# Kernel tuning notes

Measured on AMD Instinct MI355X. Metric: run time of the kernel, lower is better.

## Reference

```python
import jax, jax.numpy as jnp
import numpy as np

NEG = float(-2**32 + 1)  # huge negative used by the original sign-based masking
EPS = 1e-8
NUM_BLOCKS = 3
NUM_HEADS = 1


def _mha(xq, xk, xv, Wq, bq, Wk, bk, Wv, bv):
    # manual QKV with ReLU, as in the torch module
    Q = jax.nn.relu(xq @ Wq + bq)   # [B, Lq, D]
    K = jax.nn.relu(xk @ Wk + bk)   # [B, Lk, D]
    V = jax.nn.relu(xv @ Wv + bv)
    B, Lq, D = Q.shape
    Lk = K.shape[1]
    dh = D // NUM_HEADS
    Qh = Q.reshape(B, Lq, NUM_HEADS, dh)
    Kh = K.reshape(B, Lk, NUM_HEADS, dh)
    Vh = V.reshape(B, Lk, NUM_HEADS, dh)
    scores = jnp.einsum('bqhd,bkhd->bhqk', Qh, Kh) / jnp.sqrt(jnp.float32(dh))
    # sign-based key padding mask (rows whose embedding-sum is exactly 0)
    key_mask0 = (jnp.sign(jnp.abs(jnp.sum(xk, axis=-1))) == 0.0).astype(scores.dtype)  # [B, Lk]
    cond = key_mask0[:, None, None, :]
    scores = NEG * cond + scores * (1.0 - cond)
    attn = jax.nn.softmax(scores, axis=-1)
    # post-softmax query mask
    qmask = jnp.sign(jnp.abs(jnp.sum(xq, axis=-1)))  # [B, Lq]
    attn = attn * qmask[:, None, :, None]
    out = jnp.einsum('bhqk,bkhd->bqhd', attn, Vh).reshape(B, Lq, D)
    return out + xq  # residual; note: the torch mha never applies its layernorm


def _layernorm(x, g, b):
    mu = jnp.mean(x, axis=-1, keepdims=True)
    var = jnp.mean(jnp.square(x - mu), axis=-1, keepdims=True)
    return (x - mu) / jnp.sqrt(var + EPS) * g + b


def _ffn(x, W1, b1, W2, b2, g, bln):
    h = jax.nn.relu(x @ W1 + b1) @ W2 + b2
    return _layernorm(h, g, bln) + x


def setup_inputs() -> dict:
    key = jax.random.key(0)
    ks = jax.random.split(key, 9)
    B, L, V, D, NB = 4096, 50, 50000, 200, NUM_BLOCKS
    tokens = jax.random.randint(ks[0], (B, L), 0, V)
    emb = jax.random.normal(ks[1], (V, D), dtype=jnp.float32) * 0.1
    emb = emb.at[0].set(0.0)  # padding token row -> triggers sign masks
    s = 1.0 / np.sqrt(D)
    Wq = jax.random.normal(ks[2], (NB, D, D), dtype=jnp.float32) * s
    Wk = jax.random.normal(ks[3], (NB, D, D), dtype=jnp.float32) * s
    Wv = jax.random.normal(ks[4], (NB, D, D), dtype=jnp.float32) * s
    W1 = jax.random.normal(ks[5], (NB, D, D), dtype=jnp.float32) * s
    W2 = jax.random.normal(ks[6], (NB, D, D), dtype=jnp.float32) * s
    z = jnp.zeros((NB, D), dtype=jnp.float32)
    return dict(tokens=tokens, emb=emb,
                Wq=Wq, bq=z, Wk=Wk, bk=z, Wv=Wv, bv=z,
                W1=W1, b1=z, W2=W2, b2=z,
                ln_g=jnp.ones((NB, D), dtype=jnp.float32), ln_b=z)


def reference(tokens, emb, Wq, bq, Wk, bk, Wv, bv, W1, b1, W2, b2, ln_g, ln_b):
    x = emb[tokens]  # [B, L, D]
    for i in range(NUM_BLOCKS):
        x = _mha(x, x, x, Wq[i], bq[i], Wk[i], bk[i], Wv[i], bv[i])
        x = _ffn(x, W1[i], b1[i], W2[i], b2[i], ln_g[i], ln_b[i])
    return x
```

## Files before the change

### kernel.cpp

```cpp
#include <hip/hip_runtime.h>
#include <hip/hip_bf16.h>
#include <math.h>

#define LQ 50
#define DD 200
#define NBLK 3
#define NT 1024
#define NW 16

#define KC 13
#define NT32 7
#define MAT_U (KC * NT32 * 128)

#define APS 408
#define VTS 72
#define PS  136
#define SS  66

#define NEGC (-4294967295.0f)
#define SCALE 0.07071067811865475f

typedef __attribute__((ext_vector_type(4)))  float f32x4;
typedef __attribute__((ext_vector_type(16))) float f32x16;
typedef __attribute__((ext_vector_type(8)))  short s16x8;

__device__ __forceinline__ unsigned short bf16_rne(float x) {
  unsigned u = __float_as_uint(x);
  unsigned r = u + 0x7FFF + ((u >> 16) & 1);
  return (unsigned short)(r >> 16);
}
__device__ __forceinline__ float bf16_f(unsigned short h) {
  return __uint_as_float((unsigned)h << 16);
}
__device__ __forceinline__ void splitf(float x, short& h, short& l) {
  __hip_bfloat16 bh = __float2bfloat16(x);
  float hf = __bfloat162float(bh);
  __hip_bfloat16 bl = __float2bfloat16(x - hf);
  h = (short)__builtin_bit_cast(unsigned short, bh);
  l = (short)__builtin_bit_cast(unsigned short, bl);
}
__device__ __forceinline__ unsigned short bfbits(float x) {
  __hip_bfloat16 bh = __float2bfloat16(x);
  return __builtin_bit_cast(unsigned short, bh);
}
__device__ __forceinline__ float joinf(short h, short l) {
  return __bfloat162float(__builtin_bit_cast(__hip_bfloat16, (unsigned short)h)) +
         __bfloat162float(__builtin_bit_cast(__hip_bfloat16, (unsigned short)l));
}

__device__ __forceinline__ float wave_sum(float v) {
  #pragma unroll
  for (int off = 32; off > 0; off >>= 1) v += __shfl_xor(v, off, 64);
  return v;
}
__device__ __forceinline__ float wave_max(float v) {
  #pragma unroll
  for (int off = 32; off > 0; off >>= 1) v = fmaxf(v, __shfl_xor(v, off, 64));
  return v;
}

__global__ __launch_bounds__(64)
void swizzle_w(const float* __restrict__ Wq, const float* __restrict__ Wk,
               const float* __restrict__ Wv, const float* __restrict__ W1,
               const float* __restrict__ W2, unsigned short* __restrict__ wbuf)
{
  int t = blockIdx.x;
  int nt = t % NT32; t /= NT32;
  int kc = t % KC;  t /= KC;
  int mat = t;
  int layer = mat / 5, which = mat % 5;
  const float* W;
  switch (which) {
    case 0: W = Wq; break;
    case 1: W = Wk; break;
    case 2: W = Wv; break;
    case 3: W = W1; break;
    default: W = W2; break;
  }
  W += (size_t)layer * DD * DD;

  const int l = threadIdx.x;
  const int n = nt * 32 + (l & 31);
  const int kb = kc * 16 + (l >> 5) * 8;
  s16x8 vh, vl;
  #pragma unroll
  for (int j = 0; j < 8; ++j) {
    int k = kb + j;
    float w = (k < DD && n < DD) ? W[k * DD + n] : 0.0f;
    unsigned short h = bf16_rne(w);
    unsigned short lo = bf16_rne(w - bf16_f(h));
    vh[j] = (short)h;
    vl[j] = (short)lo;
  }
  size_t base = ((size_t)((mat * KC + kc) * NT32 + nt)) * 1024 + l * 8;
  *(s16x8*)(wbuf + base)       = vh;
  *(s16x8*)(wbuf + base + 512) = vl;
}

__device__ __forceinline__ void mm32_ct_pair(
    const short* __restrict__ srcp, const s16x8* __restrict__ wt,
    const float* __restrict__ bias, short* __restrict__ dstp, int nt, int lane)
{
  const int h = lane >> 5, l31 = lane & 31;
  f32x16 acc0 = (f32x16)0.f, acc1 = (f32x16)0.f;
  int r1 = 32 + l31; if (r1 >= LQ) r1 = 0;
  const short* arow0 = srcp + l31 * APS;
  const short* arow1 = srcp + r1 * APS;

  #pragma unroll 1
  for (int kc = 0; kc < KC; ++kc) {
    const s16x8* wp = wt + (size_t)(kc * NT32 + nt) * 128 + lane;
    s16x8 wh = wp[0], wl = wp[64];
    const int ch = 2 * kc + h;
    const bool ok = (ch < 25);
    {
      s16x8 ah = (s16x8)0, al = (s16x8)0;
      if (ok) { const short* p = arow0 + ch * 16; ah = *(const s16x8*)p; al = *(const s16x8*)(p + 8); }
      acc0 = __builtin_amdgcn_mfma_f32_32x32x16_bf16(wh, ah, acc0, 0, 0, 0);
      acc0 = __builtin_amdgcn_mfma_f32_32x32x16_bf16(wh, al, acc0, 0, 0, 0);
      acc0 = __builtin_amdgcn_mfma_f32_32x32x16_bf16(wl, ah, acc0, 0, 0, 0);
    }
    {
      s16x8 ah = (s16x8)0, al = (s16x8)0;
      if (ok) { const short* p = arow1 + ch * 16; ah = *(const s16x8*)p; al = *(const s16x8*)(p + 8); }
      acc1 = __builtin_amdgcn_mfma_f32_32x32x16_bf16(wh, ah, acc1, 0, 0, 0);
      acc1 = __builtin_amdgcn_mfma_f32_32x32x16_bf16(wh, al, acc1, 0, 0, 0);
      acc1 = __builtin_amdgcn_mfma_f32_32x32x16_bf16(wl, ah, acc1, 0, 0, 0);
    }
  }

  #pragma unroll
  for (int rt = 0; rt < 2; ++rt) {
    const int r = rt * 32 + l31;
    if (r < LQ) {
      #pragma unroll
      for (int q2 = 0; q2 < 4; ++q2) {
        const int nb = nt * 32 + 8 * q2 + 4 * h;
        if (nb + 3 < DD) {
          float4 bv = *(const float4*)(bias + nb);
          float v0 = fmaxf((rt ? acc1[q2*4+0] : acc0[q2*4+0]) + bv.x, 0.f);
          float v1 = fmaxf((rt ? acc1[q2*4+1] : acc0[q2*4+1]) + bv.y, 0.f);
          float v2 = fmaxf((rt ? acc1[q2*4+2] : acc0[q2*4+2]) + bv.z, 0.f);
          float v3 = fmaxf((rt ? acc1[q2*4+3] : acc0[q2*4+3]) + bv.w, 0.f);
          short h0,l0,h1,l1,h2,l2,h3,l3;
          splitf(v0,h0,l0); splitf(v1,h1,l1); splitf(v2,h2,l2); splitf(v3,h3,l3);
          uint2 ph, pl;
          ph.x = (unsigned short)h0 | ((unsigned)(unsigned short)h1 << 16);
          ph.y = (unsigned short)h2 | ((unsigned)(unsigned short)h3 << 16);
          pl.x = (unsigned short)l0 | ((unsigned)(unsigned short)l1 << 16);
          pl.y = (unsigned short)l2 | ((unsigned)(unsigned short)l3 << 16);
          short* base = dstp + r * APS + (nb >> 3) * 16 + (nb & 7);
          *(uint2*)base = ph;
          *(uint2*)(base + 8) = pl;
        }
      }
    }
  }
}

__device__ __forceinline__ void mm32_v(
    const short* __restrict__ srcp, const s16x8* __restrict__ wt,
    const float* __restrict__ bias, short* __restrict__ vtp, int nt, int lane)
{
  const int h = lane >> 5, l31 = lane & 31;
  f32x16 acc0 = (f32x16)0.f, acc1 = (f32x16)0.f;
  int r1 = 32 + l31; if (r1 >= LQ) r1 = 0;
  const short* arow0 = srcp + l31 * APS;
  const short* arow1 = srcp + r1 * APS;

  #pragma unroll 1
  for (int kc = 0; kc < KC; ++kc) {
    const s16x8* wp = wt + (size_t)(kc * NT32 + nt) * 128 + lane;
    s16x8 wh = wp[0], wl = wp[64];
    const int ch = 2 * kc + h;
    const bool ok = (ch < 25);
    {
      s16x8 ah = (s16x8)0, al = (s16x8)0;
      if (ok) { const short* p = arow0 + ch * 16; ah = *(const s16x8*)p; al = *(const s16x8*)(p + 8); }
      acc0 = __builtin_amdgcn_mfma_f32_32x32x16_bf16(ah, wh, acc0, 0, 0, 0);
      acc0 = __builtin_amdgcn_mfma_f32_32x32x16_bf16(al, wh, acc0, 0, 0, 0);
      acc0 = __builtin_amdgcn_mfma_f32_32x32x16_bf16(ah, wl, acc0, 0, 0, 0);
    }
    {
      s16x8 ah = (s16x8)0, al = (s16x8)0;
      if (ok) { const short* p = arow1 + ch * 16; ah = *(const s16x8*)p; al = *(const s16x8*)(p + 8); }
      acc1 = __builtin_amdgcn_mfma_f32_32x32x16_bf16(ah, wh, acc1, 0, 0, 0);
      acc1 = __builtin_amdgcn_mfma_f32_32x32x16_bf16(al, wh, acc1, 0, 0, 0);
      acc1 = __builtin_amdgcn_mfma_f32_32x32x16_bf16(ah, wl, acc1, 0, 0, 0);
    }
  }

  const int d = nt * 32 + l31;
  if (d < DD) {
    const float bvs = bias[d];
    #pragma unroll
    for (int mt2 = 0; mt2 < 2; ++mt2) {
      #pragma unroll
      for (int q2 = 0; q2 < 4; ++q2) {
        const int rb = mt2 * 32 + 8 * q2 + 4 * h;
        float vv[4];
        #pragma unroll
        for (int e = 0; e < 4; ++e) {
          const int r = rb + e;
          float v = (mt2 ? acc1[q2*4+e] : acc0[q2*4+e]) + bvs;
          vv[e] = (r < LQ) ? fmaxf(v, 0.f) : 0.f;
        }
        uint2 pk;
        pk.x = (unsigned)bfbits(vv[0]) | ((unsigned)bfbits(vv[1]) << 16);
        pk.y = (unsigned)bfbits(vv[2]) | ((unsigned)bfbits(vv[3]) << 16);
        *(uint2*)(vtp + d * VTS + (rb >> 3) * 8 + (rb & 7)) = pk;
      }
    }
  }
}

__device__ __forceinline__ void mm32_w1(
    const short* __restrict__ srcp, const s16x8* __restrict__ wt,
    const float* __restrict__ bias, short* __restrict__ dstp,
    int nt, int rt, int lane)
{
  const int h = lane >> 5, l31 = lane & 31;
  f32x16 acc = (f32x16)0.f;
  int r = rt * 32 + l31;
  int rr = (r >= LQ) ? 0 : r;
  const short* arow = srcp + rr * APS;

  const s16x8* wp = wt + (size_t)nt * 128 + lane;
  s16x8 wh = wp[0], wl = wp[64];
  #pragma unroll 1
  for (int kc = 0; kc < KC; ++kc) {
    s16x8 nh = (s16x8)0, nl = (s16x8)0;
    if (kc + 1 < KC) {
      const s16x8* np = wt + (size_t)((kc + 1) * NT32 + nt) * 128 + lane;
      nh = np[0]; nl = np[64];
    }
    const int ch = 2 * kc + h;
    s16x8 ah = (s16x8)0, al = (s16x8)0;
    if (ch < 25) { const short* p = arow + ch * 16; ah = *(const s16x8*)p; al = *(const s16x8*)(p + 8); }
    acc = __builtin_amdgcn_mfma_f32_32x32x16_bf16(wh, ah, acc, 0, 0, 0);
    acc = __builtin_amdgcn_mfma_f32_32x32x16_bf16(wh, al, acc, 0, 0, 0);
    acc = __builtin_amdgcn_mfma_f32_32x32x16_bf16(wl, ah, acc, 0, 0, 0);
    wh = nh; wl = nl;
  }

  if (r < LQ) {
    #pragma unroll
    for (int q2 = 0; q2 < 4; ++q2) {
      const int nb = nt * 32 + 8 * q2 + 4 * h;
      if (nb + 3 < DD) {
        float4 bv = *(const float4*)(bias + nb);
        float v0 = fmaxf(acc[q2*4+0] + bv.x, 0.f);
        float v1 = fmaxf(acc[q2*4+1] + bv.y, 0.f);
        float v2 = fmaxf(acc[q2*4+2] + bv.z, 0.f);
        float v3 = fmaxf(acc[q2*4+3] + bv.w, 0.f);
        uint2 ph;
        ph.x = (unsigned)bfbits(v0) | ((unsigned)bfbits(v1) << 16);
        ph.y = (unsigned)bfbits(v2) | ((unsigned)bfbits(v3) << 16);
        *(uint2*)(dstp + r * APS + (nb >> 3) * 16 + (nb & 7)) = ph;
      }
    }
  }
}

__device__ __forceinline__ void mm32_w2(
    const short* __restrict__ srcp, const s16x8* __restrict__ wt,
    const float* __restrict__ bias, float* __restrict__ dstf,
    int nt, int rt, int lane)
{
  const int h = lane >> 5, l31 = lane & 31;
  f32x16 acc = (f32x16)0.f;
  int r = rt * 32 + l31;
  int rr = (r >= LQ) ? 0 : r;
  const short* arow = srcp + rr * APS;

  const s16x8* wp = wt + (size_t)nt * 128 + lane;
  s16x8 wh = wp[0], wl = wp[64];
  #pragma unroll 1
  for (int kc = 0; kc < KC; ++kc) {
    s16x8 nh = (s16x8)0, nl = (s16x8)0;
    if (kc + 1 < KC) {
      const s16x8* np = wt + (size_t)((kc + 1) * NT32 + nt) * 128 + lane;
      nh = np[0]; nl = np[64];
    }
    const int ch = 2 * kc + h;
    s16x8 ah = (s16x8)0;
    if (ch < 25) ah = *(const s16x8*)(arow + ch * 16);
    acc = __builtin_amdgcn_mfma_f32_32x32x16_bf16(wh, ah, acc, 0, 0, 0);
    acc = __builtin_amdgcn_mfma_f32_32x32x16_bf16(wl, ah, acc, 0, 0, 0);
    wh = nh; wl = nl;
  }

  if (r < LQ) {
    #pragma unroll
    for (int q2 = 0; q2 < 4; ++q2) {
      const int d0 = nt * 32 + 8 * q2 + 4 * h;
      if (d0 + 3 < DD) {
        float4 bv = *(const float4*)(bias + d0);
        float4 w4;
        w4.x = acc[q2*4+0] + bv.x; w4.y = acc[q2*4+1] + bv.y;
        w4.z = acc[q2*4+2] + bv.z; w4.w = acc[q2*4+3] + bv.w;
        *(float4*)(dstf + r * DD + d0) = w4;
      }
    }
  }
}

__global__ __launch_bounds__(NT)
void transformer_kernel(const int* __restrict__ tokens,
                        const float* __restrict__ emb,
                        const unsigned short* __restrict__ wbuf,
                        const float* __restrict__ bq, const float* __restrict__ bk,
                        const float* __restrict__ bv, const float* __restrict__ b1,
                        const float* __restrict__ b2,
                        const float* __restrict__ lng, const float* __restrict__ lnb,
                        float* __restrict__ out)
{
  __shared__ __align__(16) short xs_p[LQ * APS];
  __shared__ __align__(16) short q_p [LQ * APS];
  __shared__ __align__(16) short k_p [LQ * APS];
  __shared__ __align__(16) short vt_p[DD * VTS];
  __shared__ float rowsum[52];

  float* Sf  = (float*)q_p;
  short* Pp  = q_p + 8192;
  float* h2f = (float*)k_p;

  const int b    = blockIdx.x;
  const int tid  = threadIdx.x;
  const int lane = tid & 63;
  const int wv   = tid >> 6;
  const int g    = lane >> 4, c = lane & 15;

  for (int o = tid; o < LQ * 25; o += NT) {
    int r = o / 25, ch = o % 25;
    int tok = tokens[b * LQ + r];
    const float* ep = emb + (size_t)tok * DD + ch * 8;
    float4 a0 = *(const float4*)ep;
    float4 a1 = *(const float4*)(ep + 4);
    float xv[8] = {a0.x, a0.y, a0.z, a0.w, a1.x, a1.y, a1.z, a1.w};
    s16x8 hh, ll;
    #pragma unroll
    for (int j = 0; j < 8; ++j) { short h, l; splitf(xv[j], h, l); hh[j] = h; ll[j] = l; }
    short* dp = xs_p + r * APS + ch * 16;
    *(s16x8*)dp = hh;
    *(s16x8*)(dp + 8) = ll;
  }
  __syncthreads();

  for (int layer = 0; layer < NBLK; ++layer) {
    const s16x8* wq  = (const s16x8*)wbuf + (size_t)(layer * 5 + 0) * MAT_U;
    const s16x8* wk  = (const s16x8*)wbuf + (size_t)(layer * 5 + 1) * MAT_U;
    const s16x8* wvv = (const s16x8*)wbuf + (size_t)(layer * 5 + 2) * MAT_U;
    const s16x8* w1  = (const s16x8*)wbuf + (size_t)(layer * 5 + 3) * MAT_U;
    const s16x8* w2  = (const s16x8*)wbuf + (size_t)(layer * 5 + 4) * MAT_U;
    const float* bql = bq + layer * DD;
    const float* bkl = bk + layer * DD;
    const float* bvl = bv + layer * DD;
    const float* b1l = b1 + layer * DD;
    const float* b2l = b2 + layer * DD;
    const float* gl  = lng + layer * DD;
    const float* bl  = lnb + layer * DD;

    if (layer == 0) {
      for (int r = wv; r < LQ; r += NW) {
        float s = 0.f;
        #pragma unroll
        for (int t = 0; t < 4; ++t) {
          int cc = lane + 64 * t;
          if (cc < DD) {
            const short* p = xs_p + r * APS + (cc >> 3) * 16 + (cc & 7);
            s += joinf(p[0], p[8]);
          }
        }
        s = wave_sum(s);
        if (lane == 0) rowsum[r] = s;
      }
    }

    if (wv < 7)                      mm32_ct_pair(xs_p, wq, bql, q_p, wv, lane);
    else if (wv >= 8 && wv < 15)     mm32_ct_pair(xs_p, wk, bkl, k_p, wv - 8, lane);
    __syncthreads();

    f32x4 s0 = (f32x4)0.f, s1 = (f32x4)0.f;
    if (wv >= 8) {
      const int w8 = wv - 8;
      const int mt = w8 >> 1;
      const int nk0 = (w8 & 1) * 2;
      int qr = mt * 16 + c;          if (qr >= LQ) qr = 0;
      int kj0 = nk0 * 16 + c;        if (kj0 >= LQ) kj0 = 0;
      int kj1 = (nk0 + 1) * 16 + c;  if (kj1 >= LQ) kj1 = 0;
      const short* qrow = q_p + qr * APS;
      const short* k0r  = k_p + kj0 * APS;
      const short* k1r  = k_p + kj1 * APS;
      #pragma unroll 1
      for (int kt = 0; kt < 7; ++kt) {
        const int ch = kt * 4 + g;
        s16x8 qh = (s16x8)0, ql = (s16x8)0;
        s16x8 kh0 = (s16x8)0, kl0 = (s16x8)0, kh1 = (s16x8)0, kl1 = (s16x8)0;
        if (ch < 25) {
          qh  = *(const s16x8*)(qrow + ch * 16); ql  = *(const s16x8*)(qrow + ch * 16 + 8);
          kh0 = *(const s16x8*)(k0r + ch * 16);  kl0 = *(const s16x8*)(k0r + ch * 16 + 8);
          kh1 = *(const s16x8*)(k1r + ch * 16);  kl1 = *(const s16x8*)(k1r + ch * 16 + 8);
        }
        s0 = __builtin_amdgcn_mfma_f32_16x16x32_bf16(qh, kh0, s0, 0, 0, 0);
        s0 = __builtin_amdgcn_mfma_f32_16x16x32_bf16(ql, kh0, s0, 0, 0, 0);
        s0 = __builtin_amdgcn_mfma_f32_16x16x32_bf16(qh, kl0, s0, 0, 0, 0);
        s1 = __builtin_amdgcn_mfma_f32_16x16x32_bf16(qh, kh1, s1, 0, 0, 0);
        s1 = __builtin_amdgcn_mfma_f32_16x16x32_bf16(ql, kh1, s1, 0, 0, 0);
        s1 = __builtin_amdgcn_mfma_f32_16x16x32_bf16(qh, kl1, s1, 0, 0, 0);
      }
    } else if (wv < 7) {
      mm32_v(xs_p, wvv, bvl, vt_p, wv, lane);
    }
    __syncthreads();

    if (wv >= 8) {
      const int w8 = wv - 8;
      const int mt = w8 >> 1;
      const int nk0 = (w8 & 1) * 2;
      #pragma unroll
      for (int t = 0; t < 2; ++t) {
        const int j = (nk0 + t) * 16 + c;
        const f32x4 sa = t ? s1 : s0;
        const bool km = (j < LQ) && (rowsum[j] != 0.0f);
        #pragma unroll
        for (int q = 0; q < 4; ++q) {
          const int qi = mt * 16 + g * 4 + q;
          if (qi < LQ) Sf[qi * SS + j] = km ? sa[q] * SCALE : NEGC;
        }
      }
    }
    __syncthreads();

    for (int r = wv; r < LQ; r += NW) {
      float sm = -INFINITY;
      if (lane < LQ) sm = Sf[r * SS + lane];
      float m = wave_max(sm);
      float e = (lane < LQ) ? __expf(sm - m) : 0.0f;
      float ssum = wave_sum(e);
      float qm = (rowsum[r] == 0.0f) ? 0.0f : 1.0f;
      float a = e / ssum * qm;
      Pp[r * PS + (lane >> 3) * 16 + (lane & 7)] = (short)bfbits(a);
    }
    __syncthreads();

    if (wv < 13) {
      const int mt = wv;
      f32x4 pa[4];
      #pragma unroll
      for (int nq = 0; nq < 4; ++nq) pa[nq] = (f32x4)0.f;
      int vr = mt * 16 + c; if (vr >= DD) vr = 0;
      const short* vrow = vt_p + vr * VTS;
      #pragma unroll
      for (int kt = 0; kt < 2; ++kt) {
        s16x8 vh = *(const s16x8*)(vrow + (kt * 4 + g) * 8);
        #pragma unroll
        for (int nq = 0; nq < 4; ++nq) {
          int pr = nq * 16 + c; if (pr >= LQ) pr = 0;
          s16x8 pbh = *(const s16x8*)(Pp + pr * PS + (kt * 4 + g) * 16);
          pa[nq] = __builtin_amdgcn_mfma_f32_16x16x32_bf16(vh, pbh, pa[nq], 0, 0, 0);
        }
      }
      const int d0 = mt * 16 + g * 4;
      if (d0 + 3 < DD) {
        #pragma unroll
        for (int nq = 0; nq < 4; ++nq) {
          const int qq = nq * 16 + c;
          if (qq < LQ) {
            short* base = xs_p + qq * APS + (d0 >> 3) * 16 + (d0 & 7);
            uint2 ph = *(const uint2*)base;
            uint2 pl = *(const uint2*)(base + 8);
            float f0 = joinf((short)(ph.x & 0xFFFF), (short)(pl.x & 0xFFFF)) + pa[nq][0];
            float f1 = joinf((short)(ph.x >> 16),    (short)(pl.x >> 16))    + pa[nq][1];
            float f2 = joinf((short)(ph.y & 0xFFFF), (short)(pl.y & 0xFFFF)) + pa[nq][2];
            float f3 = joinf((short)(ph.y >> 16),    (short)(pl.y >> 16))    + pa[nq][3];
            short h0,l0,h1,l1,h2,l2,h3,l3;
            splitf(f0,h0,l0); splitf(f1,h1,l1); splitf(f2,h2,l2); splitf(f3,h3,l3);
            ph.x = (unsigned short)h0 | ((unsigned)(unsigned short)h1 << 16);
            ph.y = (unsigned short)h2 | ((unsigned)(unsigned short)h3 << 16);
            pl.x = (unsigned short)l0 | ((unsigned)(unsigned short)l1 << 16);
            pl.y = (unsigned short)l2 | ((unsigned)(unsigned short)l3 << 16);
            *(uint2*)base = ph;
            *(uint2*)(base + 8) = pl;
          }
        }
      }
    }
    __syncthreads();

    if (wv < 14) mm32_w1(xs_p, w1, b1l, q_p, wv >> 1, wv & 1, lane);
    __syncthreads();
    if (wv < 14) mm32_w2(q_p, w2, b2l, h2f, wv >> 1, wv & 1, lane);
    __syncthreads();

    for (int r = wv; r < LQ; r += NW) {
      float hv[4];
      #pragma unroll
      for (int t = 0; t < 4; ++t) {
        int cc = lane + 64 * t;
        hv[t] = (cc < DD) ? h2f[r * DD + cc] : 0.f;
      }
      float mu = wave_sum(hv[0] + hv[1] + hv[2] + hv[3]) * (1.0f / 200.0f);
      float d0 = hv[0] - mu, d1 = hv[1] - mu, d2 = hv[2] - mu;
      float d3 = (lane + 192 < DD) ? (hv[3] - mu) : 0.f;
      float var = wave_sum(d0 * d0 + d1 * d1 + d2 * d2 + d3 * d3) * (1.0f / 200.0f);
      float inv = 1.0f / sqrtf(var + 1e-8f);
      float dd4[4] = {d0, d1, d2, d3};
      float rs = 0.f;
      #pragma unroll
      for (int t = 0; t < 4; ++t) {
        int cc = lane + 64 * t;
        if (cc < DD) {
          short* hp = xs_p + r * APS + (cc >> 3) * 16 + (cc & 7);
          float nv = dd4[t] * inv * gl[cc] + bl[cc] + joinf(hp[0], hp[8]);
          rs += nv;
          short h, l; splitf(nv, h, l);
          hp[0] = h; hp[8] = l;
        }
      }
      rs = wave_sum(rs);
      if (lane == 0) rowsum[r] = rs;
    }
    __syncthreads();
  }

  for (int o = tid; o < LQ * 25; o += NT) {
    int r = o / 25, ch = o % 25;
    const short* sp = xs_p + r * APS + ch * 16;
    s16x8 hh = *(const s16x8*)sp;
    s16x8 ll = *(const s16x8*)(sp + 8);
    float4 o0, o1;
    o0.x = joinf(hh[0], ll[0]); o0.y = joinf(hh[1], ll[1]);
    o0.z = joinf(hh[2], ll[2]); o0.w = joinf(hh[3], ll[3]);
    o1.x = joinf(hh[4], ll[4]); o1.y = joinf(hh[5], ll[5]);
    o1.z = joinf(hh[6], ll[6]); o1.w = joinf(hh[7], ll[7]);
    float* op = out + ((size_t)b * LQ + r) * DD + ch * 8;
    *(float4*)op = o0;
    *(float4*)(op + 4) = o1;
  }
}

extern "C" void kernel_launch(void* const* d_in, const int* in_sizes, int n_in,
                              void* d_out, int out_size, void* d_ws, size_t ws_size,
                              hipStream_t stream) {
  const int*   tokens = (const int*)  d_in[0];
  const float* emb    = (const float*)d_in[1];
  const float* Wq     = (const float*)d_in[2];
  const float* bq     = (const float*)d_in[3];
  const float* Wk     = (const float*)d_in[4];
  const float* bk     = (const float*)d_in[5];
  const float* Wv     = (const float*)d_in[6];
  const float* bv     = (const float*)d_in[7];
  const float* W1     = (const float*)d_in[8];
  const float* b1     = (const float*)d_in[9];
  const float* W2     = (const float*)d_in[10];
  const float* b2     = (const float*)d_in[11];
  const float* lng    = (const float*)d_in[12];
  const float* lnb    = (const float*)d_in[13];
  float* out = (float*)d_out;
  unsigned short* wbuf = (unsigned short*)d_ws;

  hipLaunchKernelGGL(swizzle_w, dim3(15 * KC * NT32), dim3(64), 0, stream,
                     Wq, Wk, Wv, W1, W2, wbuf);

  const int B = in_sizes[0] / LQ;
  hipLaunchKernelGGL(transformer_kernel, dim3(B), dim3(NT), 0, stream,
                     tokens, emb, wbuf, bq, bk, bv, b1, b2, lng, lnb, out);
}
```

Baseline: 1.664 ms.

## Fuse Q/K projections per wave and run V alongside, spread scores over all waves

Q and K projections are now computed together in one loop per wave, reusing the same activation fragment loads, while the V projection runs concurrently on the other seven waves. The score computation is redistributed so all 16 waves each compute one 16x16 tile, and scores get their own shared buffer, removing one barrier-separated phase. VTS padding shrinks to free shared memory for the new score buffer. This rebalances work across the schedule but raises accumulator register pressure in the fused QK routine and increases LDS usage.

```diff
diff --git a/kernel.cpp b/kernel.cpp
--- a/kernel.cpp
+++ b/kernel.cpp
@@ -13,7 +13,7 @@
 #define MAT_U (KC * NT32 * 128)
 
 #define APS 408
-#define VTS 72
+#define VTS 66
 #define PS  136
 #define SS  66
 
@@ -97,38 +97,10 @@
   *(s16x8*)(wbuf + base + 512) = vl;
 }
 
-__device__ __forceinline__ void mm32_ct_pair(
-    const short* __restrict__ srcp, const s16x8* __restrict__ wt,
-    const float* __restrict__ bias, short* __restrict__ dstp, int nt, int lane)
-{
-  const int h = lane >> 5, l31 = lane & 31;
-  f32x16 acc0 = (f32x16)0.f, acc1 = (f32x16)0.f;
-  int r1 = 32 + l31; if (r1 >= LQ) r1 = 0;
-  const short* arow0 = srcp + l31 * APS;
-  const short* arow1 = srcp + r1 * APS;
-
-  #pragma unroll 1
-  for (int kc = 0; kc < KC; ++kc) {
-    const s16x8* wp = wt + (size_t)(kc * NT32 + nt) * 128 + lane;
-    s16x8 wh = wp[0], wl = wp[64];
-    const int ch = 2 * kc + h;
-    const bool ok = (ch < 25);
-    {
-      s16x8 ah = (s16x8)0, al = (s16x8)0;
-      if (ok) { const short* p = arow0 + ch * 16; ah = *(const s16x8*)p; al = *(const s16x8*)(p + 8); }
-      acc0 = __builtin_amdgcn_mfma_f32_32x32x16_bf16(wh, ah, acc0, 0, 0, 0);
-      acc0 = __builtin_amdgcn_mfma_f32_32x32x16_bf16(wh, al, acc0, 0, 0, 0);
-      acc0 = __builtin_amdgcn_mfma_f32_32x32x16_bf16(wl, ah, acc0, 0, 0, 0);
-    }
-    {
-      s16x8 ah = (s16x8)0, al = (s16x8)0;
-      if (ok) { const short* p = arow1 + ch * 16; ah = *(const s16x8*)p; al = *(const s16x8*)(p + 8); }
-      acc1 = __builtin_amdgcn_mfma_f32_32x32x16_bf16(wh, ah, acc1, 0, 0, 0);
-      acc1 = __builtin_amdgcn_mfma_f32_32x32x16_bf16(wh, al, acc1, 0, 0, 0);
-      acc1 = __builtin_amdgcn_mfma_f32_32x32x16_bf16(wl, ah, acc1, 0, 0, 0);
-    }
-  }
-
+__device__ __forceinline__ void store_ct_pair(
+    const f32x16& acc0, const f32x16& acc1, const float* __restrict__ bias,
+    short* __restrict__ dstp, int nt, int h, int l31)
+{
   #pragma unroll
   for (int rt = 0; rt < 2; ++rt) {
     const int r = rt * 32 + l31;
@@ -158,6 +130,52 @@
   }
 }
 
+__device__ __forceinline__ void mm32_qkf(
+    const short* __restrict__ srcp,
+    const s16x8* __restrict__ wtq, const s16x8* __restrict__ wtk,
+    const float* __restrict__ bq, const float* __restrict__ bk,
+    short* __restrict__ dq, short* __restrict__ dk, int nt, int lane)
+{
+  const int h = lane >> 5, l31 = lane & 31;
+  f32x16 aQ0 = (f32x16)0.f, aQ1 = (f32x16)0.f;
+  f32x16 aK0 = (f32x16)0.f, aK1 = (f32x16)0.f;
+  int r1 = 32 + l31; if (r1 >= LQ) r1 = 0;
+  const short* arow0 = srcp + l31 * APS;
+  const short* arow1 = srcp + r1 * APS;
+
+  #pragma unroll 1
+  for (int kc = 0; kc < KC; ++kc) {
+    const s16x8* wpq = wtq + (size_t)(kc * NT32 + nt) * 128 + lane;
+    const s16x8* wpk = wtk + (size_t)(kc * NT32 + nt) * 128 + lane;
+    s16x8 wqh = wpq[0], wql = wpq[64];
+    s16x8 wkh = wpk[0], wkl = wpk[64];
+    const int ch = 2 * kc + h;
+    const bool ok = (ch < 25);
+    {
+      s16x8 ah = (s16x8)0, al = (s16x8)0;
+      if (ok) { const short* p = arow0 + ch * 16; ah = *(const s16x8*)p; al = *(const s16x8*)(p + 8); }
+      aQ0 = __builtin_amdgcn_mfma_f32_32x32x16_bf16(wqh, ah, aQ0, 0, 0, 0);
+      aQ0 = __builtin_amdgcn_mfma_f32_32x32x16_bf16(wqh, al, aQ0, 0, 0, 0);
+      aQ0 = __builtin_amdgcn_mfma_f32_32x32x16_bf16(wql, ah, aQ0, 0, 0, 0);
+      aK0 = __builtin_amdgcn_mfma_f32_32x32x16_bf16(wkh, ah, aK0, 0, 0, 0);
+      aK0 = __builtin_amdgcn_mfma_f32_32x32x16_bf16(wkh, al, aK0, 0, 0, 0);
+      aK0 = __builtin_amdgcn_mfma_f32_32x32x16_bf16(wkl, ah, aK0, 0, 0, 0);
+    }
+    {
+      s16x8 ah = (s16x8)0, al = (s16x8)0;
+      if (ok) { const short* p = arow1 + ch * 16; ah = *(const s16x8*)p; al = *(const s16x8*)(p + 8); }
+      aQ1 = __builtin_amdgcn_mfma_f32_32x32x16_bf16(wqh, ah, aQ1, 0, 0, 0);
+      aQ1 = __builtin_amdgcn_mfma_f32_32x32x16_bf16(wqh, al, aQ1, 0, 0, 0);
+      aQ1 = __builtin_amdgcn_mfma_f32_32x32x16_bf16(wql, ah, aQ1, 0, 0, 0);
+      aK1 = __builtin_amdgcn_mfma_f32_32x32x16_bf16(wkh, ah, aK1, 0, 0, 0);
+      aK1 = __builtin_amdgcn_mfma_f32_32x32x16_bf16(wkh, al, aK1, 0, 0, 0);
+      aK1 = __builtin_amdgcn_mfma_f32_32x32x16_bf16(wkl, ah, aK1, 0, 0, 0);
+    }
+  }
+  store_ct_pair(aQ0, aQ1, bq, dq, nt, h, l31);
+  store_ct_pair(aK0, aK1, bk, dk, nt, h, l31);
+}
+
 __device__ __forceinline__ void mm32_v(
     const short* __restrict__ srcp, const s16x8* __restrict__ wt,
     const float* __restrict__ bias, short* __restrict__ vtp, int nt, int lane)
@@ -319,10 +337,10 @@
   __shared__ __align__(16) short q_p [LQ * APS];
   __shared__ __align__(16) short k_p [LQ * APS];
   __shared__ __align__(16) short vt_p[DD * VTS];
+  __shared__ __align__(16) float Sf[LQ * SS];
   __shared__ float rowsum[52];
 
-  float* Sf  = (float*)q_p;
-  short* Pp  = q_p + 8192;
+  short* Pp  = q_p;
   float* h2f = (float*)k_p;
 
   const int b    = blockIdx.x;
@@ -377,57 +395,37 @@
       }
     }
 
-    if (wv < 7)                      mm32_ct_pair(xs_p, wq, bql, q_p, wv, lane);
-    else if (wv >= 8 && wv < 15)     mm32_ct_pair(xs_p, wk, bkl, k_p, wv - 8, lane);
-    __syncthreads();
-
-    f32x4 s0 = (f32x4)0.f, s1 = (f32x4)0.f;
-    if (wv >= 8) {
-      const int w8 = wv - 8;
-      const int mt = w8 >> 1;
-      const int nk0 = (w8 & 1) * 2;
-      int qr = mt * 16 + c;          if (qr >= LQ) qr = 0;
-      int kj0 = nk0 * 16 + c;        if (kj0 >= LQ) kj0 = 0;
-      int kj1 = (nk0 + 1) * 16 + c;  if (kj1 >= LQ) kj1 = 0;
+    if (wv < 7)                   mm32_qkf(xs_p, wq, wk, bql, bkl, q_p, k_p, wv, lane);
+    else if (wv >= 8 && wv < 15)  mm32_v(xs_p, wvv, bvl, vt_p, wv - 8, lane);
+    __syncthreads();
+
+    {
+      const int mt  = wv >> 2;
+      const int ntk = wv & 3;
+      f32x4 s0 = (f32x4)0.f;
+      int qr = mt * 16 + c;   if (qr >= LQ) qr = 0;
+      int kj = ntk * 16 + c;  if (kj >= LQ) kj = 0;
       const short* qrow = q_p + qr * APS;
-      const short* k0r  = k_p + kj0 * APS;
-      const short* k1r  = k_p + kj1 * APS;
+      const short* k0r  = k_p + kj * APS;
       #pragma unroll 1
       for (int kt = 0; kt < 7; ++kt) {
         const int ch = kt * 4 + g;
         s16x8 qh = (s16x8)0, ql = (s16x8)0;
-        s16x8 kh0 = (s16x8)0, kl0 = (s16x8)0, kh1 = (s16x8)0, kl1 = (s16x8)0;
+        s16x8 kh0 = (s16x8)0, kl0 = (s16x8)0;
         if (ch < 25) {
           qh  = *(const s16x8*)(qrow + ch * 16); ql  = *(const s16x8*)(qrow + ch * 16 + 8);
           kh0 = *(const s16x8*)(k0r + ch * 16);  kl0 = *(const s16x8*)(k0r + ch * 16 + 8);
-          kh1 = *(const s16x8*)(k1r + ch * 16);  kl1 = *(const s16x8*)(k1r + ch * 16 + 8);
         }
         s0 = __builtin_amdgcn_mfma_f32_16x16x32_bf16(qh, kh0, s0, 0, 0, 0);
         s0 = __builtin_amdgcn_mfma_f32_16x16x32_bf16(ql, kh0, s0, 0, 0, 0);
         s0 = __builtin_amdgcn_mfma_f32_16x16x32_bf16(qh, kl0, s0, 0, 0, 0);
-        s1 = __builtin_amdgcn_mfma_f32_16x16x32_bf16(qh, kh1, s1, 0, 0, 0);
-        s1 = __builtin_amdgcn_mfma_f32_16x16x32_bf16(ql, kh1, s1, 0, 0, 0);
-        s1 = __builtin_amdgcn_mfma_f32_16x16x32_bf16(qh, kl1, s1, 0, 0, 0);
-      }
-    } else if (wv < 7) {
-      mm32_v(xs_p, wvv, bvl, vt_p, wv, lane);
-    }
-    __syncthreads();
-
-    if (wv >= 8) {
-      const int w8 = wv - 8;
-      const int mt = w8 >> 1;
-      const int nk0 = (w8 & 1) * 2;
-      #pragma unroll
-      for (int t = 0; t < 2; ++t) {
-        const int j = (nk0 + t) * 16 + c;
-        const f32x4 sa = t ? s1 : s0;
-        const bool km = (j < LQ) && (rowsum[j] != 0.0f);
-        #pragma unroll
-        for (int q = 0; q < 4; ++q) {
-          const int qi = mt * 16 + g * 4 + q;
-          if (qi < LQ) Sf[qi * SS + j] = km ? sa[q] * SCALE : NEGC;
-        }
+      }
+      const int j = ntk * 16 + c;
+      const bool km = (j < LQ) && (rowsum[j] != 0.0f);
+      #pragma unroll
+      for (int q = 0; q < 4; ++q) {
+        const int qi = mt * 16 + g * 4 + q;
+        if (qi < LQ) Sf[qi * SS + j] = km ? s0[q] * SCALE : NEGC;
       }
     }
     __syncthreads();
```

After: 1.855 ms. 1.11x slower.
